# Optimization experiments

Hardware: AMD Instinct MI355X
Metric: run time of the kernel (lower is better)

## Reference

```python
import jax, jax.numpy as jnp
import numpy as np

LAYERS = 3
DILATION = 2
RES_NORM = 1.0 / np.sqrt(2.0).astype(np.float32)
NEG_SLOPE = 0.2
T, B, D = 256, 128, 1024


def setup_inputs() -> dict:
    key = jax.random.key(0)
    k0, k1, k2, k3, k4 = jax.random.split(key, 5)
    s = 1.0 / np.sqrt(D)  # torch GRUCell default init bound
    x = jax.random.normal(k0, (1, T, B, D), dtype=jnp.float32)
    W_ih = jax.random.uniform(k1, (LAYERS, 3 * D, D), jnp.float32, -s, s)
    W_hh = jax.random.uniform(k2, (LAYERS, 3 * D, D), jnp.float32, -s, s)
    b_ih = jax.random.uniform(k3, (LAYERS, 3 * D), jnp.float32, -s, s)
    b_hh = jax.random.uniform(k4, (LAYERS, 3 * D), jnp.float32, -s, s)
    return {"x": x, "W_ih": W_ih, "W_hh": W_hh, "b_ih": b_ih, "b_hh": b_hh}


def _gru_cell(x, h, W_ih, W_hh, b_ih, b_hh):
    # torch.nn.GRUCell math
    gi = x @ W_ih.T + b_ih  # [B, 3D]
    gh = h @ W_hh.T + b_hh  # [B, 3D]
    i_r, i_z, i_n = jnp.split(gi, 3, axis=-1)
    h_r, h_z, h_n = jnp.split(gh, 3, axis=-1)
    r = jax.nn.sigmoid(i_r + h_r)
    z = jax.nn.sigmoid(i_z + h_z)
    n = jnp.tanh(i_n + r * h_n)
    return (1.0 - z) * n + z * h


def reference(x, W_ih, W_hh, b_ih, b_hh):
    xs = x[0]  # squeeze(0) -> [T, B, D]
    b, d = xs.shape[1], xs.shape[2]
    # dilated hidden buffers: layer l keeps DILATION**l past hiddens (init None -> zeros)
    bufs0 = tuple(jnp.zeros((DILATION ** l, b, d), xs.dtype) for l in range(LAYERS))

    def step(bufs, x_t):
        h_in = x_t
        new_bufs = []
        for l in range(LAYERS):
            h_out = _gru_cell(h_in, bufs[l][0], W_ih[l], W_hh[l], b_ih[l], b_hh[l])
            # append h_out, pop oldest (roll buffer)
            new_bufs.append(jnp.concatenate([bufs[l][1:], h_out[None]], axis=0))
            # layers > 1 -> dilated residual + LeakyReLU(0.2), scaled by 1/sqrt(2)
            h_in = jax.nn.leaky_relu((h_out + h_in) * RES_NORM, negative_slope=NEG_SLOPE)
        return tuple(new_bufs), h_in

    _, outs = jax.lax.scan(step, bufs0, xs)  # outs: [T, B, D]
    return outs[None]  # unsqueeze(0) -> [1, T, B, D]
```

## Files before the change

### kernel.cpp

```cpp
#include <hip/hip_runtime.h>
#include <hip/hip_bf16.h>

#define TT 256
#define D 1024
#define BD (128 * 1024)
#define NWPL 85
#define NWG 256
#define NUSED 255
#define ROWLEN 1048

typedef __attribute__((ext_vector_type(8))) short bf16x8;
typedef __attribute__((ext_vector_type(4))) float f32x4;

__device__ __forceinline__ unsigned short f2bf(float f) {
    __hip_bfloat16 h = __float2bfloat16(f);
    return *reinterpret_cast<unsigned short*>(&h);
}
__device__ __forceinline__ float bf2f(unsigned short u) {
    unsigned v = (unsigned)u << 16;
    return __builtin_bit_cast(float, v);
}

__global__ __launch_bounds__(256) void cvt_f32_bf16(const float* __restrict__ in,
                                                    unsigned short* __restrict__ out, int n) {
    int i = (blockIdx.x * 256 + threadIdx.x) * 8;
    if (i + 8 <= n) {
        float4 a = *(const float4*)(in + i);
        float4 b = *(const float4*)(in + i + 4);
        unsigned short t[8] = { f2bf(a.x), f2bf(a.y), f2bf(a.z), f2bf(a.w),
                                f2bf(b.x), f2bf(b.y), f2bf(b.z), f2bf(b.w) };
        *(uint4*)(out + i) = *(const uint4*)t;
    }
}

__global__ __launch_bounds__(512, 2) void dgru_dataflow(
    const unsigned short* __restrict__ xbf,
    const float* __restrict__ Wih, const float* __restrict__ Whh,
    const float* __restrict__ bih, const float* __restrict__ bhh,
    unsigned short* __restrict__ ring_bf,
    float* __restrict__ ring_f,
    unsigned short* __restrict__ hin_ring,
    float* __restrict__ out,
    unsigned* __restrict__ prog)
{
    __shared__ unsigned short wlds[78 * ROWLEN];

    const int grp = blockIdx.x & 7;
    const int p = 32 * grp + (blockIdx.x >> 3);
    if (p >= NUSED) return;
    const int layer = p / NWPL;
    const int u     = p % NWPL;
    const int ncols = (u < 4) ? 13 : 12;
    const int c0    = u * 12 + (u < 4 ? u : 4);

    const int tid = threadIdx.x;

    {
        const float* w0 = Wih + (size_t)layer * 3 * D * D;
        const float* w1 = Whh + (size_t)layer * 3 * D * D;
        const int nrows = 6 * ncols;
        const int rh   = tid >> 8;
        const int t255 = tid & 255;
        for (int rid = rh; rid < nrows; rid += 2) {
            int m   = rid / (3 * ncols);
            int rem = rid - m * 3 * ncols;
            int g   = rem / ncols;
            int c   = rem - g * ncols;
            const float* src = (m ? w1 : w0) + ((size_t)g * D + c0 + c) * D + t255 * 4;
            float4 v = *(const float4*)src;
            ushort4 o = { f2bf(v.x), f2bf(v.y), f2bf(v.z), f2bf(v.w) };
            *(ushort4*)&wlds[rid * ROWLEN + t255 * 4] = o;
        }
        __syncthreads();
    }

    const int wave = tid >> 6;
    const int lane = tid & 63;
    const int r15  = lane & 15;
    const int kq   = lane >> 4;
    const int kq8  = kq * 8;
    const int c_cl = (r15 < ncols) ? r15 : (ncols - 1);
    const bool cvalid = r15 < ncols;
    const int col  = c0 + c_cl;

    const float bi2 = bih[layer * 3 * D + 2 * D + col];
    const float bh2 = bhh[layer * 3 * D + 2 * D + col];
    const float bs0 = bih[layer * 3 * D + col] + bhh[layer * 3 * D + col];
    const float bs1 = bih[layer * 3 * D + D + col] + bhh[layer * 3 * D + D + col];

    const unsigned short* bp[6];
    #pragma unroll
    for (int mg = 0; mg < 6; ++mg) bp[mg] = wlds + (mg * ncols + c_cl) * ROWLEN;

    const int arow_off = (wave * 16 + r15) * D;

    const int dil = 1 << layer;

    unsigned* pr0 = prog;
    unsigned* pr1 = prog + 128;
    unsigned* pr2 = prog + 256;
    unsigned* myflag = prog + layer * 128 + u;

    const int j2 = (lane < 21) ? lane + 64 : lane;

    for (int t = 0; t < TT; ++t) {
        int th1, th2, th3; unsigned *a1, *a2, *a3;
        if (layer == 0)      { a1 = pr0; th1 = t;     a2 = pr1; th2 = t - 30; a3 = pr2; th3 = 0;      }
        else if (layer == 1) { a1 = pr0; th1 = t + 1; a2 = pr1; th2 = t - 1;  a3 = pr2; th3 = t - 30; }
        else                 { a1 = pr1; th1 = t + 1; a2 = pr2; th2 = t - 3;  a3 = pr2; th3 = 0;      }

        if (wave == 0) {
            for (;;) {
                bool ok = true;
                if (th1 > 0) ok = ok && (int)__hip_atomic_load(a1 + lane, __ATOMIC_RELAXED, __HIP_MEMORY_SCOPE_AGENT) >= th1
                                     && (int)__hip_atomic_load(a1 + j2,   __ATOMIC_RELAXED, __HIP_MEMORY_SCOPE_AGENT) >= th1;
                if (th2 > 0) ok = ok && (int)__hip_atomic_load(a2 + lane, __ATOMIC_RELAXED, __HIP_MEMORY_SCOPE_AGENT) >= th2
                                     && (int)__hip_atomic_load(a2 + j2,   __ATOMIC_RELAXED, __HIP_MEMORY_SCOPE_AGENT) >= th2;
                if (th3 > 0) ok = ok && (int)__hip_atomic_load(a3 + lane, __ATOMIC_RELAXED, __HIP_MEMORY_SCOPE_AGENT) >= th3
                                     && (int)__hip_atomic_load(a3 + j2,   __ATOMIC_RELAXED, __HIP_MEMORY_SCOPE_AGENT) >= th3;
                if (__all(ok)) break;
                __builtin_amdgcn_s_sleep(1);
            }
            if ((t & 15) == 0)
                __builtin_amdgcn_fence(__ATOMIC_ACQUIRE, "agent");
        }
        __syncthreads();

        const unsigned short* hinb = layer ? hin_ring + (size_t)((layer - 1) * 32 + (t & 31)) * BD
                                           : xbf + (size_t)t * BD;
        const int rs = (t + 32 - dil) & 31, wsl = t & 31;
        const unsigned short* hprevb = ring_bf + (size_t)(layer * 32 + rs) * BD;
        const float*  hprevf = ring_f + (size_t)(layer * 32 + rs) * BD;
        float*        houtf  = ring_f + (size_t)(layer * 32 + wsl) * BD;
        unsigned short* houtb = ring_bf + (size_t)(layer * 32 + wsl) * BD;

        float hpv[4], rsv[4];
        #pragma unroll
        for (int q = 0; q < 4; ++q) {
            const int row = wave * 16 + kq * 4 + q;
            const size_t idx = (size_t)row * D + col;
            hpv[q] = hprevf[idx];
            rsv[q] = bf2f(hinb[idx]);
        }

        f32x4 acc[2][3] = {};
        bf16x8 A0[8], A1[8], A2[8];

#define ISSUE1(Av, KS, SL) { \
        Av[(SL) * 2 + 0] = *(const bf16x8*)(hinb   + arow_off + (KS) * 32 + kq8); \
        Av[(SL) * 2 + 1] = *(const bf16x8*)(hprevb + arow_off + (KS) * 32 + kq8); }
#define ISSUEG(Av, BASE) { ISSUE1(Av, (BASE) + 0, 0) ISSUE1(Av, (BASE) + 1, 1) \
                           ISSUE1(Av, (BASE) + 2, 2) ISSUE1(Av, (BASE) + 3, 3) \
                           __builtin_amdgcn_sched_barrier(0); }
#define COMPG(Av, BASE) { _Pragma("unroll") for (int kk = 0; kk < 4; ++kk) { \
        bf16x8 Bv[6]; \
        _Pragma("unroll") for (int mg = 0; mg < 6; ++mg) \
            Bv[mg] = *(const bf16x8*)(bp[mg] + ((BASE) + kk) * 32 + kq8); \
        _Pragma("unroll") for (int g = 0; g < 3; ++g) { \
            acc[0][g] = __builtin_amdgcn_mfma_f32_16x16x32_bf16(Av[kk * 2 + 0], Bv[g],     acc[0][g], 0, 0, 0); \
            acc[1][g] = __builtin_amdgcn_mfma_f32_16x16x32_bf16(Av[kk * 2 + 1], Bv[3 + g], acc[1][g], 0, 0, 0); } } \
        __builtin_amdgcn_sched_barrier(0); }

        ISSUEG(A0, 0);  ISSUEG(A1, 4);  ISSUEG(A2, 8);
        COMPG(A0, 0);   ISSUEG(A0, 12);
        COMPG(A1, 4);   ISSUEG(A1, 16);
        COMPG(A2, 8);   ISSUEG(A2, 20);
        COMPG(A0, 12);  ISSUEG(A0, 24);
        COMPG(A1, 16);  ISSUEG(A1, 28);
        COMPG(A2, 20);
        COMPG(A0, 24);
        COMPG(A1, 28);

        #pragma unroll
        for (int q = 0; q < 4; ++q) {
            const int row = wave * 16 + kq * 4 + q;
            const size_t idx = (size_t)row * D + col;
            float xr = acc[0][0][q] + acc[1][0][q] + bs0;
            float xz = acc[0][1][q] + acc[1][1][q] + bs1;
            float rg = 1.f / (1.f + __expf(-xr));
            float zg = 1.f / (1.f + __expf(-xz));
            float ng = tanhf(acc[0][2][q] + bi2 + rg * (acc[1][2][q] + bh2));
            float hp = hpv[q];
            float h  = (1.f - zg) * ng + zg * hp;
            float v = (h + rsv[q]) * 0.70710678f;
            float y = v > 0.f ? v : 0.2f * v;
            if (cvalid) {
                houtf[idx] = h;
                houtb[idx] = f2bf(h);
                if (layer == 2) {
                    out[(size_t)t * BD + idx] = y;
                } else {
                    hin_ring[(size_t)(layer * 32 + (t & 31)) * BD + idx] = f2bf(y);
                }
            }
        }

        __syncthreads();
        if (tid == 0) {
            __builtin_amdgcn_fence(__ATOMIC_RELEASE, "agent");
            __hip_atomic_store(myflag, (unsigned)(t + 1), __ATOMIC_RELAXED, __HIP_MEMORY_SCOPE_AGENT);
        }
    }
}

extern "C" void kernel_launch(void* const* d_in, const int* in_sizes, int n_in,
                              void* d_out, int out_size, void* d_ws, size_t ws_size,
                              hipStream_t stream) {
    const float* x   = (const float*)d_in[0];
    const float* Wih = (const float*)d_in[1];
    const float* Whh = (const float*)d_in[2];
    const float* bih = (const float*)d_in[3];
    const float* bhh = (const float*)d_in[4];
    float* out = (float*)d_out;

    char* ws = (char*)d_ws;
    size_t off = 0;
    auto alloc = [&](size_t bytes) -> void* {
        void* p = ws + off;
        off += (bytes + 255) & ~(size_t)255;
        return p;
    };

    const int NX = TT * BD;
    unsigned short* xbf = (unsigned short*)alloc((size_t)NX * 2);

    size_t zstart = off;
    unsigned short* ring_bf  = (unsigned short*)alloc((size_t)96 * BD * 2);
    float*          ring_f   = (float*)alloc((size_t)96 * BD * 4);
    unsigned short* hin_ring = (unsigned short*)alloc((size_t)64 * BD * 2);
    unsigned*       prog     = (unsigned*)alloc(2048);
    size_t zbytes = off - zstart;

    cvt_f32_bf16<<<NX / 8 / 256, 256, 0, stream>>>(x, xbf, NX);
    hipMemsetAsync(ws + zstart, 0, zbytes, stream);

    dgru_dataflow<<<NWG, 512, 0, stream>>>(
        xbf, Wih, Whh, bih, bhh,
        ring_bf, ring_f, hin_ring, out,
        prog);
}
```

Measured before the change: 6.446 ms.

## Shrink ring buffers to 8 slots and use coherent sc0/sc1 loads instead of acquire fences

Cuts the inter-layer ring buffers from 32 to 8 slots and tightens the back-pressure thresholds to match, which shrinks the working set so it can stay closer to the caches. The periodic agent-scope acquire fence is removed. Activation loads now go through inline-asm global loads with sc0 sc1 cache-bypass bits, and stores become relaxed agent-scope atomics, so cross-workgroup visibility comes from the cache policy. The A-operand prefetch grows to four register groups with explicit vmcnt waits, adding register pressure and relying on hand-counted wait values being correct.

Measured after the change: 5.768 ms. 1.12x faster.

```diff
diff --git a/kernel.cpp b/kernel.cpp
--- a/kernel.cpp
+++ b/kernel.cpp
@@ -32,6 +32,19 @@
         *(uint4*)(out + i) = *(const uint4*)t;
     }
 }
+
+#define GLSC16(dst, base, IMM) asm volatile( \
+    "global_load_dwordx4 %0, %1, off offset:%2 sc0 sc1" \
+    : "=v"(dst) : "v"(base), "i"(IMM))
+#define GLSCD(dst, addr) asm volatile( \
+    "global_load_dword %0, %1, off sc0 sc1" : "=v"(dst) : "v"(addr))
+#define GLSCU(dst, addr) asm volatile( \
+    "global_load_ushort %0, %1, off sc0 sc1" : "=v"(dst) : "v"(addr))
+#define WAITV(N) { asm volatile("s_waitcnt vmcnt(%0)" :: "i"(N)); \
+                   __builtin_amdgcn_sched_barrier(0); }
+#define SB __builtin_amdgcn_sched_barrier(0)
+#define AGLD(p) __hip_atomic_load((p), __ATOMIC_RELAXED, __HIP_MEMORY_SCOPE_AGENT)
+#define AGST(p, v) __hip_atomic_store((p), (v), __ATOMIC_RELAXED, __HIP_MEMORY_SCOPE_AGENT)
 
 __global__ __launch_bounds__(512, 2) void dgru_dataflow(
     const unsigned short* __restrict__ xbf,
@@ -92,7 +105,7 @@
     #pragma unroll
     for (int mg = 0; mg < 6; ++mg) bp[mg] = wlds + (mg * ncols + c_cl) * ROWLEN;
 
-    const int arow_off = (wave * 16 + r15) * D;
+    const int arow_off = (wave * 16 + r15) * D + kq8;
 
     const int dil = 1 << layer;
 
@@ -105,53 +118,54 @@
 
     for (int t = 0; t < TT; ++t) {
         int th1, th2, th3; unsigned *a1, *a2, *a3;
-        if (layer == 0)      { a1 = pr0; th1 = t;     a2 = pr1; th2 = t - 30; a3 = pr2; th3 = 0;      }
-        else if (layer == 1) { a1 = pr0; th1 = t + 1; a2 = pr1; th2 = t - 1;  a3 = pr2; th3 = t - 30; }
-        else                 { a1 = pr1; th1 = t + 1; a2 = pr2; th2 = t - 3;  a3 = pr2; th3 = 0;      }
+        if (layer == 0)      { a1 = pr0; th1 = t;     a2 = pr1; th2 = t - 7; a3 = pr2; th3 = 0;     }
+        else if (layer == 1) { a1 = pr0; th1 = t + 1; a2 = pr1; th2 = t - 1; a3 = pr2; th3 = t - 7; }
+        else                 { a1 = pr1; th1 = t + 1; a2 = pr2; th2 = t - 3; a3 = pr2; th3 = 0;     }
 
         if (wave == 0) {
             for (;;) {
                 bool ok = true;
-                if (th1 > 0) ok = ok && (int)__hip_atomic_load(a1 + lane, __ATOMIC_RELAXED, __HIP_MEMORY_SCOPE_AGENT) >= th1
-                                     && (int)__hip_atomic_load(a1 + j2,   __ATOMIC_RELAXED, __HIP_MEMORY_SCOPE_AGENT) >= th1;
-                if (th2 > 0) ok = ok && (int)__hip_atomic_load(a2 + lane, __ATOMIC_RELAXED, __HIP_MEMORY_SCOPE_AGENT) >= th2
-                                     && (int)__hip_atomic_load(a2 + j2,   __ATOMIC_RELAXED, __HIP_MEMORY_SCOPE_AGENT) >= th2;
-                if (th3 > 0) ok = ok && (int)__hip_atomic_load(a3 + lane, __ATOMIC_RELAXED, __HIP_MEMORY_SCOPE_AGENT) >= th3
-                                     && (int)__hip_atomic_load(a3 + j2,   __ATOMIC_RELAXED, __HIP_MEMORY_SCOPE_AGENT) >= th3;
+                if (th1 > 0) ok = ok && (int)AGLD(a1 + lane) >= th1 && (int)AGLD(a1 + j2) >= th1;
+                if (th2 > 0) ok = ok && (int)AGLD(a2 + lane) >= th2 && (int)AGLD(a2 + j2) >= th2;
+                if (th3 > 0) ok = ok && (int)AGLD(a3 + lane) >= th3 && (int)AGLD(a3 + j2) >= th3;
                 if (__all(ok)) break;
                 __builtin_amdgcn_s_sleep(1);
             }
-            if ((t & 15) == 0)
-                __builtin_amdgcn_fence(__ATOMIC_ACQUIRE, "agent");
         }
         __syncthreads();
 
-        const unsigned short* hinb = layer ? hin_ring + (size_t)((layer - 1) * 32 + (t & 31)) * BD
+        const unsigned short* hinb = layer ? hin_ring + (size_t)((layer - 1) * 8 + (t & 7)) * BD
                                            : xbf + (size_t)t * BD;
-        const int rs = (t + 32 - dil) & 31, wsl = t & 31;
-        const unsigned short* hprevb = ring_bf + (size_t)(layer * 32 + rs) * BD;
-        const float*  hprevf = ring_f + (size_t)(layer * 32 + rs) * BD;
-        float*        houtf  = ring_f + (size_t)(layer * 32 + wsl) * BD;
-        unsigned short* houtb = ring_bf + (size_t)(layer * 32 + wsl) * BD;
-
-        float hpv[4], rsv[4];
-        #pragma unroll
-        for (int q = 0; q < 4; ++q) {
-            const int row = wave * 16 + kq * 4 + q;
-            const size_t idx = (size_t)row * D + col;
-            hpv[q] = hprevf[idx];
-            rsv[q] = bf2f(hinb[idx]);
+        const int rs = (t + 8 - dil) & 7, wsl = t & 7;
+        const unsigned short* hprevb = ring_bf + (size_t)(layer * 8 + rs) * BD;
+        const float*  hprevf = ring_f + (size_t)(layer * 8 + rs) * BD;
+        float*        houtf  = ring_f + (size_t)(layer * 8 + wsl) * BD;
+        unsigned short* houtb = ring_bf + (size_t)(layer * 8 + wsl) * BD;
+
+        const unsigned short* ba_h = hinb + arow_off;
+        const unsigned short* ba_p = hprevb + arow_off;
+
+        float hpv[4]; unsigned ru[4];
+        {
+            #pragma unroll
+            for (int q = 0; q < 4; ++q) {
+                const int row = wave * 16 + kq * 4 + q;
+                const size_t idx = (size_t)row * D + col;
+                GLSCD(hpv[q], hprevf + idx);
+                GLSCU(ru[q], hinb + idx);
+            }
+            SB;
         }
 
         f32x4 acc[2][3] = {};
-        bf16x8 A0[8], A1[8], A2[8];
+        bf16x8 A0[8], A1[8], A2[8], A3[8];
 
 #define ISSUE1(Av, KS, SL) { \
-        Av[(SL) * 2 + 0] = *(const bf16x8*)(hinb   + arow_off + (KS) * 32 + kq8); \
-        Av[(SL) * 2 + 1] = *(const bf16x8*)(hprevb + arow_off + (KS) * 32 + kq8); }
+        GLSC16(Av[(SL) * 2 + 0], ba_h, (KS) * 64); \
+        GLSC16(Av[(SL) * 2 + 1], ba_p, (KS) * 64); }
 #define ISSUEG(Av, BASE) { ISSUE1(Av, (BASE) + 0, 0) ISSUE1(Av, (BASE) + 1, 1) \
                            ISSUE1(Av, (BASE) + 2, 2) ISSUE1(Av, (BASE) + 3, 3) \
-                           __builtin_amdgcn_sched_barrier(0); }
+                           SB; }
 #define COMPG(Av, BASE) { _Pragma("unroll") for (int kk = 0; kk < 4; ++kk) { \
         bf16x8 Bv[6]; \
         _Pragma("unroll") for (int mg = 0; mg < 6; ++mg) \
@@ -159,17 +173,17 @@
         _Pragma("unroll") for (int g = 0; g < 3; ++g) { \
             acc[0][g] = __builtin_amdgcn_mfma_f32_16x16x32_bf16(Av[kk * 2 + 0], Bv[g],     acc[0][g], 0, 0, 0); \
             acc[1][g] = __builtin_amdgcn_mfma_f32_16x16x32_bf16(Av[kk * 2 + 1], Bv[3 + g], acc[1][g], 0, 0, 0); } } \
-        __builtin_amdgcn_sched_barrier(0); }
-
-        ISSUEG(A0, 0);  ISSUEG(A1, 4);  ISSUEG(A2, 8);
-        COMPG(A0, 0);   ISSUEG(A0, 12);
-        COMPG(A1, 4);   ISSUEG(A1, 16);
-        COMPG(A2, 8);   ISSUEG(A2, 20);
-        COMPG(A0, 12);  ISSUEG(A0, 24);
-        COMPG(A1, 16);  ISSUEG(A1, 28);
-        COMPG(A2, 20);
-        COMPG(A0, 24);
-        COMPG(A1, 28);
+        SB; }
+
+        ISSUEG(A0, 0); ISSUEG(A1, 4); ISSUEG(A2, 8); ISSUEG(A3, 12);
+        WAITV(24); COMPG(A0, 0);  ISSUEG(A0, 16);
+        WAITV(24); COMPG(A1, 4);  ISSUEG(A1, 20);
+        WAITV(24); COMPG(A2, 8);  ISSUEG(A2, 24);
+        WAITV(24); COMPG(A3, 12); ISSUEG(A3, 28);
+        WAITV(24); COMPG(A0, 16);
+        WAITV(16); COMPG(A1, 20);
+        WAITV(8);  COMPG(A2, 24);
+        WAITV(0);  COMPG(A3, 28);
 
         #pragma unroll
         for (int q = 0; q < 4; ++q) {
@@ -182,23 +196,24 @@
             float ng = tanhf(acc[0][2][q] + bi2 + rg * (acc[1][2][q] + bh2));
             float hp = hpv[q];
             float h  = (1.f - zg) * ng + zg * hp;
-            float v = (h + rsv[q]) * 0.70710678f;
+            float v = (h + bf2f((unsigned short)ru[q])) * 0.70710678f;
             float y = v > 0.f ? v : 0.2f * v;
             if (cvalid) {
-                houtf[idx] = h;
-                houtb[idx] = f2bf(h);
+                AGST(&houtf[idx], h);
+                AGST(&houtb[idx], f2bf(h));
                 if (layer == 2) {
-                    out[(size_t)t * BD + idx] = y;
+                    AGST(&out[(size_t)t * BD + idx], y);
                 } else {
-                    hin_ring[(size_t)(layer * 32 + (t & 31)) * BD + idx] = f2bf(y);
+                    AGST(&hin_ring[(size_t)(layer * 8 + (t & 7)) * BD + idx], f2bf(y));
                 }
             }
         }
 
+        asm volatile("s_waitcnt vmcnt(0)");
         __syncthreads();
         if (tid == 0) {
             __builtin_amdgcn_fence(__ATOMIC_RELEASE, "agent");
-            __hip_atomic_store(myflag, (unsigned)(t + 1), __ATOMIC_RELAXED, __HIP_MEMORY_SCOPE_AGENT);
+            AGST(myflag, (unsigned)(t + 1));
         }
     }
 }
@@ -225,9 +240,9 @@
     unsigned short* xbf = (unsigned short*)alloc((size_t)NX * 2);
 
     size_t zstart = off;
-    unsigned short* ring_bf  = (unsigned short*)alloc((size_t)96 * BD * 2);
-    float*          ring_f   = (float*)alloc((size_t)96 * BD * 4);
-    unsigned short* hin_ring = (unsigned short*)alloc((size_t)64 * BD * 2);
+    unsigned short* ring_bf  = (unsigned short*)alloc((size_t)24 * BD * 2);
+    float*          ring_f   = (float*)alloc((size_t)24 * BD * 4);
+    unsigned short* hin_ring = (unsigned short*)alloc((size_t)16 * BD * 2);
     unsigned*       prog     = (unsigned*)alloc(2048);
     size_t zbytes = off - zstart;
 
```
